# Optimization experiments

Measured on AMD Instinct MI355X. Metric: run time of the kernel, lower is better.

## Reference

```python
import jax, jax.numpy as jnp
import numpy as np

B, T, C = 4, 2048, 768   # batch, seq, n_embd
E, K = 8, 2              # n_routed_experts, moe_top_k (expert hidden dim == C per source)


def setup_inputs() -> dict:
    key = jax.random.key(0)
    ks = jax.random.split(key, 6)
    s = 0.02  # init scale to keep relu(x)^2 well-behaved
    return {
        "x": jax.random.normal(ks[0], (B, T, C), jnp.float32),
        "w_fc_sh": jax.random.normal(ks[1], (C, C), jnp.float32) * s,    # shared expert c_fc (stored [in,out])
        "w_proj_sh": jax.random.normal(ks[2], (C, C), jnp.float32) * s,  # shared expert c_proj
        "w1": jax.random.normal(ks[3], (E, C, C), jnp.float32) * s,      # routed experts c_fc, [E,in,out]
        "w2": jax.random.normal(ks[4], (E, C, C), jnp.float32) * s,      # routed experts c_proj
        "router_w": jax.random.normal(ks[5], (E, C), jnp.float32) * s,   # router weight [E, C]
        "balance_bias": jnp.zeros((E,), jnp.float32),                    # router balance_bias buffer
    }


def _mlp(x, wfc, wproj):
    # MLP: c_proj(relu(c_fc(x))**2)
    h = jnp.square(jax.nn.relu(x @ wfc))
    return h @ wproj


def reference(x, w_fc_sh, w_proj_sh, w1, w2, router_w, balance_bias):
    Bx, Tx, Cx = x.shape
    shared = _mlp(x, w_fc_sh, w_proj_sh)                    # [B,T,C]

    xf = x.reshape(-1, Cx)                                  # [N,C]
    # --- router ---
    logits = xf.astype(jnp.float32) @ router_w.T            # [N,E]
    scores = jax.nn.sigmoid(logits)
    _, idx = jax.lax.top_k(scores + balance_bias, K)        # selection uses biased scores
    tw = jnp.take_along_axis(scores, idx, axis=-1)          # gate weights from unbiased scores
    tw = tw / (tw.sum(-1, keepdims=True) + 1e-20)           # [N,K]

    # per-token per-expert combine weights (equivalent to gather/MLP/index_add loop)
    combine = (jax.nn.one_hot(idx, E, dtype=tw.dtype) * tw[..., None]).sum(1)  # [N,E]

    # dense all-expert compute, masked combine (same math as sparse dispatch)
    h = jnp.square(jax.nn.relu(jnp.einsum('nc,ech->neh', xf, w1)))  # [N,E,H]
    y = jnp.einsum('neh,ehc->nec', h, w2)                            # [N,E,C]
    routed = jnp.einsum('nec,ne->nc', y, combine)                    # [N,C]

    return shared + routed.reshape(Bx, Tx, Cx)
```

## Files before the change

### kernel.cpp

```cpp
#include <hip/hip_runtime.h>
#include <stdint.h>

#define N_TOK 8192
#define C_DIM 768
#define E_NUM 8
#define NTK 24
#define GRIDG 624
#define PREP_WT 10368
#define PREP_TOT (PREP_WT + N_TOK / 4)

typedef short short8 __attribute__((ext_vector_type(8)));
typedef __bf16 bf16x8 __attribute__((ext_vector_type(8)));
typedef float f32x4 __attribute__((ext_vector_type(4)));

static __device__ __forceinline__ unsigned short f2bf(float f) {
    unsigned u = __float_as_uint(f);
    unsigned r = u + 0x7FFFu + ((u >> 16) & 1u);
    return (unsigned short)(r >> 16);
}
static __device__ __forceinline__ float bf2f(unsigned short h) {
    return __uint_as_float(((unsigned)h) << 16);
}

__global__ __launch_bounds__(256) void prep_kernel(const float* __restrict__ wfc,
                                                   const float* __restrict__ wpj,
                                                   const float* __restrict__ w1,
                                                   const float* __restrict__ w2,
                                                   unsigned short* __restrict__ Wt,
                                                   const float* __restrict__ x,
                                                   const float* __restrict__ rw,
                                                   const float* __restrict__ bias,
                                                   float* __restrict__ topk_w,
                                                   int* __restrict__ eids,
                                                   unsigned short* __restrict__ xb) {
    __shared__ float tile[32][33];
    const int bx = blockIdx.x;
    const int t = threadIdx.x;
    if (bx < PREP_WT) {
        const int m = bx / 576;
        const int rem = bx - m * 576;
        const int i0 = (rem / 24) * 32;
        const int o0 = (rem % 24) * 32;
        const int tx = t & 31, ty = t >> 5;
        const float* src = (m == 0) ? wfc : (m == 1) ? wpj
                         : (m < 10) ? (w1 + (size_t)(m - 2) * C_DIM * C_DIM)
                                    : (w2 + (size_t)(m - 10) * C_DIM * C_DIM);
        #pragma unroll
        for (int rr = 0; rr < 32; rr += 8)
            tile[ty + rr][tx] = src[(size_t)(i0 + ty + rr) * C_DIM + o0 + tx];
        __syncthreads();
        unsigned short* dst = Wt + (size_t)m * C_DIM * C_DIM;
        #pragma unroll
        for (int rr = 0; rr < 32; rr += 8) {
            int o = o0 + ty + rr;
            dst[(size_t)o * C_DIM + i0 + tx] = f2bf(tile[tx][ty + rr]);
        }
    } else {
        const int rb = bx - PREP_WT;
        const int wave = t >> 6;
        const int lane = t & 63;
        const int n = rb * 4 + wave;
        const float* xp = x + (size_t)n * C_DIM + lane * 12;
        float xv[12];
        #pragma unroll
        for (int j = 0; j < 12; j++) xv[j] = xp[j];
        unsigned short* xbp = xb + (size_t)n * C_DIM + lane * 12;
        #pragma unroll
        for (int j = 0; j < 12; j++) xbp[j] = f2bf(xv[j]);
        float acc[E_NUM];
        #pragma unroll
        for (int e = 0; e < E_NUM; e++) acc[e] = 0.f;
        #pragma unroll
        for (int e = 0; e < E_NUM; e++) {
            const float* wp = rw + (size_t)e * C_DIM + lane * 12;
            #pragma unroll
            for (int j = 0; j < 12; j++) acc[e] += xv[j] * wp[j];
        }
        #pragma unroll
        for (int e = 0; e < E_NUM; e++) {
            #pragma unroll
            for (int off = 32; off > 0; off >>= 1) acc[e] += __shfl_xor(acc[e], off, 64);
        }
        if (lane == 0) {
            float sc[E_NUM];
            #pragma unroll
            for (int e = 0; e < E_NUM; e++) sc[e] = 1.f / (1.f + expf(-acc[e]));
            int e0 = 0; float best = -1e30f;
            #pragma unroll
            for (int e = 0; e < E_NUM; e++) { float v = sc[e] + bias[e]; if (v > best) { best = v; e0 = e; } }
            int e1 = -1; float best1 = -1e30f;
            #pragma unroll
            for (int e = 0; e < E_NUM; e++) { if (e == e0) continue; float v = sc[e] + bias[e]; if (v > best1) { best1 = v; e1 = e; } }
            float w0 = sc[e0], w1 = sc[e1];
            float s = w0 + w1 + 1e-20f;
            w0 /= s; w1 /= s;
            topk_w[n * 2] = w0; topk_w[n * 2 + 1] = w1;
            eids[n * 2] = e0; eids[n * 2 + 1] = e1;
        }
    }
}

__global__ __launch_bounds__(1024) void bucketize_kernel(const int* __restrict__ eids,
                                                         int* __restrict__ counts,
                                                         int* __restrict__ buckets) {
    const int e = blockIdx.x;
    const int t = threadIdx.x;
    const int wv = t >> 6, lane = t & 63;
    __shared__ int wave_tot[16];
    int running = 0;
    for (int start = 0; start < 2 * N_TOK; start += 1024) {
        const int i = start + t;
        const int f = (eids[i] == e) ? 1 : 0;
        unsigned long long mask = __ballot(f);
        int pre = __popcll(mask & ((1ull << lane) - 1ull));
        if (lane == 0) wave_tot[wv] = __popcll(mask);
        __syncthreads();
        int wbase = 0, tot = 0;
        #pragma unroll
        for (int j = 0; j < 16; j++) { int c = wave_tot[j]; tot += c; if (j < wv) wbase += c; }
        if (f) buckets[e * N_TOK + running + wbase + pre] = i;
        running += tot;
        __syncthreads();
    }
    if (t == 0) counts[e] = running;
}

#define GLOAD_LDS(g, l) __builtin_amdgcn_global_load_lds((const __attribute__((address_space(1))) void*)(g), (__attribute__((address_space(3))) void*)(l), 16, 0, 0)
#define WAITVM0() asm volatile("s_waitcnt vmcnt(0)" ::: "memory")
#define SCHEDB() __builtin_amdgcn_sched_barrier(0)
#define BAR() __builtin_amdgcn_s_barrier()

template <int PHASE>
__global__ __launch_bounds__(512, 4) void gemm_all_kernel(const unsigned short* __restrict__ Adir,
                                                          const unsigned short* __restrict__ Agat,
                                                          const unsigned short* __restrict__ WtAll,
                                                          void* __restrict__ dstDir,
                                                          unsigned short* __restrict__ dstGat,
                                                          const int* __restrict__ counts,
                                                          const int* __restrict__ buckets) {
    const int fid = blockIdx.x;
    const int xcd = fid & 7;
    const int i6 = fid >> 3;
    const int xx = xcd * 13 + i6 / 6;
    const int y = i6 % 6;
    int cz[E_NUM];
    #pragma unroll
    for (int zz = 0; zz < E_NUM; zz++) cz[zz] = counts[zz];
    int xo[E_NUM + 1]; int a = 0;
    #pragma unroll
    for (int zz = 0; zz < E_NUM; zz++) { xo[zz] = a; a += (cz[zz] + 255) >> 8; }
    xo[E_NUM] = a;
    if (xx >= a + 32) return;
    const bool sh = (xx >= a);
    int z = 0, xl = xx - a;
    if (!sh) {
        #pragma unroll
        for (int zz = 0; zz < E_NUM; zz++)
            if (xx >= xo[zz] && xx < xo[zz + 1]) { z = zz; xl = xx - xo[zz]; }
    }
    const int rows = sh ? N_TOK : cz[z];
    const int r0 = xl * 256;
    const int c0 = y * 128;

    __shared__ __align__(16) unsigned short lds[2 * 12288];

    const int t = threadIdx.x;
    const int lane = t & 63;
    const int wv = t >> 6;
    const int wm = wv >> 1;
    const int wn = wv & 1;

    const int widx = sh ? (PHASE == 0 ? 0 : 1) : (PHASE == 0 ? 2 + z : 10 + z);
    const unsigned short* Bmat = WtAll + (size_t)widx * C_DIM * C_DIM;
    const int* bk = buckets + z * N_TOK;

    const int scol = (((lane & 3) ^ ((lane >> 3) & 3)) * 8);
    const int rA0 = wv * 16 + (lane >> 2);
    const int rA1 = 128 + rA0;
    int g0, g1;
    const unsigned short* Asrc;
    if (sh) {
        Asrc = Adir;
        g0 = r0 + rA0; g1 = r0 + rA1;
    } else {
        Asrc = Agat;
        int p0 = r0 + rA0, p1 = r0 + rA1;
        int e0v = bk[p0 < rows ? p0 : rows - 1];
        int e1v = bk[p1 < rows ? p1 : rows - 1];
        g0 = (PHASE == 0) ? (e0v >> 1) : e0v;
        g1 = (PHASE == 0) ? (e1v >> 1) : e1v;
    }
    const unsigned short* ap0 = Asrc + (size_t)g0 * C_DIM + scol;
    const unsigned short* ap1 = Asrc + (size_t)g1 * C_DIM + scol;
    const unsigned short* bp  = Bmat + (size_t)(c0 + rA0) * C_DIM + scol;

    f32x4 acc[4][4];
    #pragma unroll
    for (int i = 0; i < 4; i++)
        #pragma unroll
        for (int j = 0; j < 4; j++) acc[i][j] = (f32x4){0.f, 0.f, 0.f, 0.f};

    const int fr = lane & 15;
    const int fq = lane >> 4;
    const int ks = ((fq ^ ((fr >> 1) & 3)) * 8);

    GLOAD_LDS(ap0, lds + wv * 512 + lane * 8);
    GLOAD_LDS(ap1, lds + 4096 + wv * 512 + lane * 8);
    GLOAD_LDS(bp,  lds + 8192 + wv * 512 + lane * 8);

    #pragma unroll
    for (int kt = 0; kt < NTK; ++kt) {
        WAITVM0();
        BAR();
        SCHEDB();
        if (kt + 1 < NTK) {
            unsigned short* d = lds + ((kt + 1) & 1) * 12288;
            const int ko = (kt + 1) * 32;
            GLOAD_LDS(ap0 + ko, d + wv * 512 + lane * 8);
            GLOAD_LDS(ap1 + ko, d + 4096 + wv * 512 + lane * 8);
            GLOAD_LDS(bp + ko,  d + 8192 + wv * 512 + lane * 8);
        }
        SCHEDB();
        const unsigned short* buf = lds + (kt & 1) * 12288;
        short8 afr[4], bfr[4];
        #pragma unroll
        for (int i = 0; i < 4; i++)
            afr[i] = *reinterpret_cast<const short8*>(buf + (size_t)(wm * 64 + i * 16 + fr) * 32 + ks);
        #pragma unroll
        for (int j = 0; j < 4; j++)
            bfr[j] = *reinterpret_cast<const short8*>(buf + 8192 + (size_t)(wn * 64 + j * 16 + fr) * 32 + ks);
        __builtin_amdgcn_s_setprio(1);
        #pragma unroll
        for (int i = 0; i < 4; i++)
            #pragma unroll
            for (int j = 0; j < 4; j++)
                acc[i][j] = __builtin_amdgcn_mfma_f32_16x16x32_bf16(
                    __builtin_bit_cast(bf16x8, afr[i]), __builtin_bit_cast(bf16x8, bfr[j]), acc[i][j], 0, 0, 0);
        __builtin_amdgcn_s_setprio(0);
    }

    const int orow = r0 + wm * 64;
    const int ocol = c0 + wn * 64;
    if (sh) {
        if constexpr (PHASE == 0) {
            unsigned short* Hd = (unsigned short*)dstDir;
            #pragma unroll
            for (int i = 0; i < 4; i++)
                #pragma unroll
                for (int rr = 0; rr < 4; rr++) {
                    size_t base = (size_t)(orow + i * 16 + fq * 4 + rr) * C_DIM;
                    #pragma unroll
                    for (int j = 0; j < 4; j++) {
                        float v = acc[i][j][rr];
                        float rl = v > 0.f ? v : 0.f;
                        Hd[base + ocol + j * 16 + fr] = f2bf(rl * rl);
                    }
                }
        } else {
            float* od = (float*)dstDir;
            #pragma unroll
            for (int i = 0; i < 4; i++)
                #pragma unroll
                for (int rr = 0; rr < 4; rr++) {
                    size_t base = (size_t)(orow + i * 16 + fq * 4 + rr) * C_DIM;
                    #pragma unroll
                    for (int j = 0; j < 4; j++)
                        od[base + ocol + j * 16 + fr] = acc[i][j][rr];
                }
        }
    } else {
        #pragma unroll
        for (int i = 0; i < 4; i++)
            #pragma unroll
            for (int rr = 0; rr < 4; rr++) {
                int pos = orow + i * 16 + fq * 4 + rr;
                if (pos < rows) {
                    int ent = bk[pos];
                    size_t base = (size_t)ent * C_DIM;
                    #pragma unroll
                    for (int j = 0; j < 4; j++) {
                        float v = acc[i][j][rr];
                        if (PHASE == 0) {
                            float rl = v > 0.f ? v : 0.f;
                            dstGat[base + ocol + j * 16 + fr] = f2bf(rl * rl);
                        } else {
                            dstGat[base + ocol + j * 16 + fr] = f2bf(v);
                        }
                    }
                }
            }
    }
}

__global__ void combine_kernel(float* __restrict__ out, const unsigned short* __restrict__ Y,
                               const float* __restrict__ tw) {
    int idx = blockIdx.x * blockDim.x + threadIdx.x;
    const int per_row = C_DIM / 4;
    if (idx >= N_TOK * per_row) return;
    int n = idx / per_row;
    int c = (idx % per_row) * 4;
    float w0 = tw[n * 2], w1 = tw[n * 2 + 1];
    const ushort4 a = *reinterpret_cast<const ushort4*>(Y + (size_t)(n * 2) * C_DIM + c);
    const ushort4 b = *reinterpret_cast<const ushort4*>(Y + (size_t)(n * 2 + 1) * C_DIM + c);
    float4* op = reinterpret_cast<float4*>(out + (size_t)n * C_DIM + c);
    float4 o = *op;
    o.x += w0 * bf2f(a.x) + w1 * bf2f(b.x);
    o.y += w0 * bf2f(a.y) + w1 * bf2f(b.y);
    o.z += w0 * bf2f(a.z) + w1 * bf2f(b.z);
    o.w += w0 * bf2f(a.w) + w1 * bf2f(b.w);
    *op = o;
}

extern "C" void kernel_launch(void* const* d_in, const int* in_sizes, int n_in,
                              void* d_out, int out_size, void* d_ws, size_t ws_size,
                              hipStream_t stream) {
    const float* x   = (const float*)d_in[0];
    const float* wfc = (const float*)d_in[1];
    const float* wpj = (const float*)d_in[2];
    const float* w1  = (const float*)d_in[3];
    const float* w2  = (const float*)d_in[4];
    const float* rw  = (const float*)d_in[5];
    const float* bias= (const float*)d_in[6];
    float* out = (float*)d_out;

    char* ws = (char*)d_ws;
    size_t off = 0;
    auto alloc = [&](size_t bytes) { void* p = ws + off; off += (bytes + 255) & ~(size_t)255; return p; };
    unsigned short* xb   = (unsigned short*)alloc((size_t)N_TOK * C_DIM * 2);
    unsigned short* Wt   = (unsigned short*)alloc((size_t)18 * C_DIM * C_DIM * 2);
    unsigned short* H    = (unsigned short*)alloc((size_t)N_TOK * 2 * C_DIM * 2);
    unsigned short* Hsh  = (unsigned short*)alloc((size_t)N_TOK * C_DIM * 2);
    unsigned short* Y    = (unsigned short*)alloc((size_t)N_TOK * 2 * C_DIM * 2);
    float* topk_w        = (float*)alloc((size_t)N_TOK * 2 * 4);
    int* counts          = (int*)alloc(256);
    int* buckets         = (int*)alloc((size_t)E_NUM * N_TOK * 4);
    int* eids            = (int*)alloc((size_t)2 * N_TOK * 4);

    prep_kernel<<<PREP_TOT, 256, 0, stream>>>(wfc, wpj, w1, w2, Wt, x, rw, bias, topk_w, eids, xb);
    bucketize_kernel<<<E_NUM, 1024, 0, stream>>>(eids, counts, buckets);

    gemm_all_kernel<0><<<GRIDG, 512, 0, stream>>>(xb, xb, Wt, Hsh, H, counts, buckets);
    gemm_all_kernel<1><<<GRIDG, 512, 0, stream>>>(Hsh, H, Wt, out, Y, counts, buckets);

    combine_kernel<<<(N_TOK * (C_DIM / 4) + 255) / 256, 256, 0, stream>>>(out, Y, topk_w);
}
```

Measured before the change: 143.2 us.

## Enlarge GEMM tiles to 256x256 with BK=64 and staged split-pipeline prefetch

The grouped expert/shared GEMM kernel moves from 256x128 output tiles with a K-step of 32 to 256x256 tiles with a K-step of 64, using 8 waves in a 2x4 layout and 8x4 accumulators per wave. Global-to-LDS loads are split into four quarter-stages interleaved with four MFMA sub-phases, with B prefetched two steps ahead and partial vmcnt waits. The work-to-block mapping now spreads the live tiles evenly across the 8 XCDs. This raises operand reuse and cuts LDS/global traffic per FLOP, at the cost of 128KB of LDS, lower occupancy (launch bound 2), fewer blocks (312), and more barriers per K-step.

```diff
diff --git a/kernel.cpp b/kernel.cpp
--- a/kernel.cpp
+++ b/kernel.cpp
@@ -4,8 +4,8 @@
 #define N_TOK 8192
 #define C_DIM 768
 #define E_NUM 8
-#define NTK 24
-#define GRIDG 624
+#define NT64 12
+#define GRIDH 312
 #define PREP_WT 10368
 #define PREP_TOT (PREP_WT + N_TOK / 4)
 
@@ -126,23 +126,40 @@
 }
 
 #define GLOAD_LDS(g, l) __builtin_amdgcn_global_load_lds((const __attribute__((address_space(1))) void*)(g), (__attribute__((address_space(3))) void*)(l), 16, 0, 0)
-#define WAITVM0() asm volatile("s_waitcnt vmcnt(0)" ::: "memory")
+#define WAITVM(n) asm volatile("s_waitcnt vmcnt(" #n ")" ::: "memory")
+#define LGKM0() asm volatile("s_waitcnt lgkmcnt(0)" ::: "memory")
 #define SCHEDB() __builtin_amdgcn_sched_barrier(0)
 #define BAR() __builtin_amdgcn_s_barrier()
 
+#define ARD(ii, I)                                                                              \
+    af[ii][0] = *reinterpret_cast<const short8*>(buf + (size_t)(arow + (I) * 16) * 64 + ks0);   \
+    af[ii][1] = *reinterpret_cast<const short8*>(buf + (size_t)(arow + (I) * 16) * 64 + ks1);
+
+#define DO_MFMA_PAIR(I0)                                                                        \
+    __builtin_amdgcn_s_setprio(1);                                                              \
+    _Pragma("unroll")                                                                           \
+    for (int ii = 0; ii < 2; ++ii) {                                                            \
+        _Pragma("unroll")                                                                       \
+        for (int j = 0; j < 4; ++j)                                                             \
+            acc[(I0) + ii][j] = __builtin_amdgcn_mfma_f32_16x16x32_bf16(                        \
+                __builtin_bit_cast(bf16x8, af[ii][0]),                                          \
+                __builtin_bit_cast(bf16x8, bfr[j][0]), acc[(I0) + ii][j], 0, 0, 0);             \
+        _Pragma("unroll")                                                                       \
+        for (int j = 0; j < 4; ++j)                                                             \
+            acc[(I0) + ii][j] = __builtin_amdgcn_mfma_f32_16x16x32_bf16(                        \
+                __builtin_bit_cast(bf16x8, af[ii][1]),                                          \
+                __builtin_bit_cast(bf16x8, bfr[j][1]), acc[(I0) + ii][j], 0, 0, 0);             \
+    }                                                                                           \
+    __builtin_amdgcn_s_setprio(0);
+
 template <int PHASE>
-__global__ __launch_bounds__(512, 4) void gemm_all_kernel(const unsigned short* __restrict__ Adir,
+__global__ __launch_bounds__(512, 2) void gemm_all_kernel(const unsigned short* __restrict__ Adir,
                                                           const unsigned short* __restrict__ Agat,
                                                           const unsigned short* __restrict__ WtAll,
                                                           void* __restrict__ dstDir,
                                                           unsigned short* __restrict__ dstGat,
                                                           const int* __restrict__ counts,
                                                           const int* __restrict__ buckets) {
-    const int fid = blockIdx.x;
-    const int xcd = fid & 7;
-    const int i6 = fid >> 3;
-    const int xx = xcd * 13 + i6 / 6;
-    const int y = i6 % 6;
     int cz[E_NUM];
     #pragma unroll
     for (int zz = 0; zz < E_NUM; zz++) cz[zz] = counts[zz];
@@ -150,7 +167,17 @@
     #pragma unroll
     for (int zz = 0; zz < E_NUM; zz++) { xo[zz] = a; a += (cz[zz] + 255) >> 8; }
     xo[E_NUM] = a;
-    if (xx >= a + 32) return;
+    const int nw = (a + 32) * 3;
+    const int fid = blockIdx.x;
+    const int xcd = fid & 7;
+    const int idx = fid >> 3;
+    const int q = nw >> 3, r8 = nw & 7;
+    const int sz = q + (xcd < r8 ? 1 : 0);
+    if (idx >= sz) return;
+    const int wid = xcd * q + (xcd < r8 ? xcd : r8) + idx;
+    const int xx = wid / 3;
+    const int y = wid - xx * 3;
+
     const bool sh = (xx >= a);
     int z = 0, xl = xx - a;
     if (!sh) {
@@ -160,92 +187,112 @@
     }
     const int rows = sh ? N_TOK : cz[z];
     const int r0 = xl * 256;
-    const int c0 = y * 128;
-
-    __shared__ __align__(16) unsigned short lds[2 * 12288];
+    const int c0 = y * 256;
+
+    __shared__ __align__(16) unsigned short lds[2 * 32768];
 
     const int t = threadIdx.x;
     const int lane = t & 63;
     const int wv = t >> 6;
-    const int wm = wv >> 1;
-    const int wn = wv & 1;
+    const int wm = wv >> 2;
+    const int wn = wv & 3;
 
     const int widx = sh ? (PHASE == 0 ? 0 : 1) : (PHASE == 0 ? 2 + z : 10 + z);
     const unsigned short* Bmat = WtAll + (size_t)widx * C_DIM * C_DIM;
     const int* bk = buckets + z * N_TOK;
 
-    const int scol = (((lane & 3) ^ ((lane >> 3) & 3)) * 8);
-    const int rA0 = wv * 16 + (lane >> 2);
-    const int rA1 = 128 + rA0;
-    int g0, g1;
-    const unsigned short* Asrc;
-    if (sh) {
-        Asrc = Adir;
-        g0 = r0 + rA0; g1 = r0 + rA1;
-    } else {
-        Asrc = Agat;
-        int p0 = r0 + rA0, p1 = r0 + rA1;
-        int e0v = bk[p0 < rows ? p0 : rows - 1];
-        int e1v = bk[p1 < rows ? p1 : rows - 1];
-        g0 = (PHASE == 0) ? (e0v >> 1) : e0v;
-        g1 = (PHASE == 0) ? (e1v >> 1) : e1v;
-    }
-    const unsigned short* ap0 = Asrc + (size_t)g0 * C_DIM + scol;
-    const unsigned short* ap1 = Asrc + (size_t)g1 * C_DIM + scol;
-    const unsigned short* bp  = Bmat + (size_t)(c0 + rA0) * C_DIM + scol;
-
-    f32x4 acc[4][4];
+    const int hr = t >> 3;
+    const int scol = (((t & 7) ^ (hr & 7)) * 8);
+    const unsigned short* ap[4];
+    const unsigned short* bp[4];
+    {
+        const unsigned short* Asrc = sh ? Adir : Agat;
+        const int rowoff[4] = {hr, 64 + hr, 128 + hr, 192 + hr};
+        #pragma unroll
+        for (int k = 0; k < 4; k++) {
+            int g;
+            if (sh) {
+                g = r0 + rowoff[k];
+            } else {
+                int p = r0 + rowoff[k];
+                int ev = bk[p < rows ? p : rows - 1];
+                g = (PHASE == 0) ? (ev >> 1) : ev;
+            }
+            ap[k] = Asrc + (size_t)g * C_DIM + scol;
+            bp[k] = Bmat + (size_t)(c0 + rowoff[k]) * C_DIM + scol;
+        }
+    }
+    auto STG = [&](int half, int kt, int db) {
+        unsigned short* d = lds + db * 32768 + half * 8192 + t * 8;
+        const unsigned short* s0 = (half < 2 ? ap[half * 2] : bp[(half - 2) * 2]) + kt * 64;
+        const unsigned short* s1 = (half < 2 ? ap[half * 2 + 1] : bp[(half - 2) * 2 + 1]) + kt * 64;
+        GLOAD_LDS(s0, d);
+        GLOAD_LDS(s1, d + 4096);
+    };
+
+    f32x4 acc[8][4];
     #pragma unroll
-    for (int i = 0; i < 4; i++)
+    for (int i = 0; i < 8; i++)
         #pragma unroll
         for (int j = 0; j < 4; j++) acc[i][j] = (f32x4){0.f, 0.f, 0.f, 0.f};
 
     const int fr = lane & 15;
     const int fq = lane >> 4;
-    const int ks = ((fq ^ ((fr >> 1) & 3)) * 8);
-
-    GLOAD_LDS(ap0, lds + wv * 512 + lane * 8);
-    GLOAD_LDS(ap1, lds + 4096 + wv * 512 + lane * 8);
-    GLOAD_LDS(bp,  lds + 8192 + wv * 512 + lane * 8);
-
-    #pragma unroll
-    for (int kt = 0; kt < NTK; ++kt) {
-        WAITVM0();
+    const int ks0 = ((fq ^ (fr & 7)) * 8);
+    const int ks1 = (((4 + fq) ^ (fr & 7)) * 8);
+    const int arow = wm * 128 + fr;
+    const int brow = wn * 64 + fr;
+
+    STG(0, 0, 0); STG(1, 0, 0); STG(2, 0, 0); STG(3, 0, 0);
+    STG(2, 1, 1); STG(3, 1, 1);
+    WAITVM(4);
+    BAR();
+
+    for (int kt = 0; kt < NT64; ++kt) {
+        const unsigned short* buf = lds + (kt & 1) * 32768;
+        const unsigned short* bbuf = buf + 16384;
+        const int nb = (kt + 1) & 1;
+        short8 bfr[4][2];
+        short8 af[2][2];
+        #pragma unroll
+        for (int j = 0; j < 4; j++) {
+            bfr[j][0] = *reinterpret_cast<const short8*>(bbuf + (size_t)(brow + j * 16) * 64 + ks0);
+            bfr[j][1] = *reinterpret_cast<const short8*>(bbuf + (size_t)(brow + j * 16) * 64 + ks1);
+        }
+        ARD(0, 0) ARD(1, 1)
+        if (kt + 1 < NT64) STG(0, kt + 1, nb);
+        BAR(); LGKM0(); SCHEDB();
+        DO_MFMA_PAIR(0)
         BAR();
-        SCHEDB();
-        if (kt + 1 < NTK) {
-            unsigned short* d = lds + ((kt + 1) & 1) * 12288;
-            const int ko = (kt + 1) * 32;
-            GLOAD_LDS(ap0 + ko, d + wv * 512 + lane * 8);
-            GLOAD_LDS(ap1 + ko, d + 4096 + wv * 512 + lane * 8);
-            GLOAD_LDS(bp + ko,  d + 8192 + wv * 512 + lane * 8);
-        }
-        SCHEDB();
-        const unsigned short* buf = lds + (kt & 1) * 12288;
-        short8 afr[4], bfr[4];
-        #pragma unroll
-        for (int i = 0; i < 4; i++)
-            afr[i] = *reinterpret_cast<const short8*>(buf + (size_t)(wm * 64 + i * 16 + fr) * 32 + ks);
-        #pragma unroll
-        for (int j = 0; j < 4; j++)
-            bfr[j] = *reinterpret_cast<const short8*>(buf + 8192 + (size_t)(wn * 64 + j * 16 + fr) * 32 + ks);
-        __builtin_amdgcn_s_setprio(1);
-        #pragma unroll
-        for (int i = 0; i < 4; i++)
-            #pragma unroll
-            for (int j = 0; j < 4; j++)
-                acc[i][j] = __builtin_amdgcn_mfma_f32_16x16x32_bf16(
-                    __builtin_bit_cast(bf16x8, afr[i]), __builtin_bit_cast(bf16x8, bfr[j]), acc[i][j], 0, 0, 0);
-        __builtin_amdgcn_s_setprio(0);
-    }
-
-    const int orow = r0 + wm * 64;
+        ARD(0, 2) ARD(1, 3)
+        if (kt + 1 < NT64) STG(1, kt + 1, nb);
+        BAR(); LGKM0(); SCHEDB();
+        DO_MFMA_PAIR(2)
+        BAR();
+        ARD(0, 4) ARD(1, 5)
+        if (kt + 2 < NT64) STG(2, kt + 2, kt & 1);
+        BAR(); LGKM0(); SCHEDB();
+        DO_MFMA_PAIR(4)
+        BAR();
+        ARD(0, 6) ARD(1, 7)
+        if (kt + 2 < NT64) {
+            STG(3, kt + 2, kt & 1);
+            WAITVM(4);
+        } else {
+            WAITVM(0);
+        }
+        BAR(); LGKM0(); SCHEDB();
+        DO_MFMA_PAIR(6)
+        BAR();
+    }
+
+    const int orow = r0 + wm * 128;
     const int ocol = c0 + wn * 64;
     if (sh) {
         if constexpr (PHASE == 0) {
             unsigned short* Hd = (unsigned short*)dstDir;
             #pragma unroll
-            for (int i = 0; i < 4; i++)
+            for (int i = 0; i < 8; i++)
                 #pragma unroll
                 for (int rr = 0; rr < 4; rr++) {
                     size_t base = (size_t)(orow + i * 16 + fq * 4 + rr) * C_DIM;
@@ -259,7 +306,7 @@
         } else {
             float* od = (float*)dstDir;
             #pragma unroll
-            for (int i = 0; i < 4; i++)
+            for (int i = 0; i < 8; i++)
                 #pragma unroll
                 for (int rr = 0; rr < 4; rr++) {
                     size_t base = (size_t)(orow + i * 16 + fq * 4 + rr) * C_DIM;
@@ -270,7 +317,7 @@
         }
     } else {
         #pragma unroll
-        for (int i = 0; i < 4; i++)
+        for (int i = 0; i < 8; i++)
             #pragma unroll
             for (int rr = 0; rr < 4; rr++) {
                 int pos = orow + i * 16 + fq * 4 + rr;
@@ -339,8 +386,8 @@
     prep_kernel<<<PREP_TOT, 256, 0, stream>>>(wfc, wpj, w1, w2, Wt, x, rw, bias, topk_w, eids, xb);
     bucketize_kernel<<<E_NUM, 1024, 0, stream>>>(eids, counts, buckets);
 
-    gemm_all_kernel<0><<<GRIDG, 512, 0, stream>>>(xb, xb, Wt, Hsh, H, counts, buckets);
-    gemm_all_kernel<1><<<GRIDG, 512, 0, stream>>>(Hsh, H, Wt, out, Y, counts, buckets);
+    gemm_all_kernel<0><<<GRIDH, 512, 0, stream>>>(xb, xb, Wt, Hsh, H, counts, buckets);
+    gemm_all_kernel<1><<<GRIDH, 512, 0, stream>>>(Hsh, H, Wt, out, Y, counts, buckets);
 
     combine_kernel<<<(N_TOK * (C_DIM / 4) + 255) / 256, 256, 0, stream>>>(out, Y, topk_w);
 }
```

Result: slower. 159.6 us (+11.5%).
